# Kernel optimization log

Hardware: AMD Instinct MI355X
Metric: run time of the kernel (lower is better)

The kernel has to match this reference:

```python
import jax, jax.numpy as jnp
import numpy as np
import math

D_MODEL = 1024
NHEAD = 16
HEAD_DIM = D_MODEL // NHEAD  # 64
R_HEAD = 8  # r // nhead = 128 // 16


def setup_inputs() -> dict:
    key = jax.random.key(0)
    ks = jax.random.split(key, 6)
    b, s = 2, 2048
    scale = 1.0 / math.sqrt(D_MODEL)
    return {
        "x": jax.random.normal(ks[0], (b, s, D_MODEL), dtype=jnp.float32),
        "Wq": jax.random.normal(ks[1], (D_MODEL, D_MODEL), dtype=jnp.float32) * scale,
        "Wk": jax.random.normal(ks[2], (D_MODEL, D_MODEL), dtype=jnp.float32) * scale,
        "Wv": jax.random.normal(ks[3], (D_MODEL, D_MODEL), dtype=jnp.float32) * scale,
        "Wo": jax.random.normal(ks[4], (D_MODEL, D_MODEL), dtype=jnp.float32) * scale,
        "B": jax.random.normal(ks[5], (D_MODEL, R_HEAD), dtype=jnp.float32),
    }


def reference(x, Wq, Wk, Wv, Wo, B):
    b, s, d = x.shape
    # Linear projections (torch nn.Linear: y = x @ W.T)
    Q = (x @ Wq.T).reshape(b, s, NHEAD, HEAD_DIM).transpose(0, 2, 1, 3)  # [b,h,s,hd]
    K = (x @ Wk.T).reshape(b, s, NHEAD, HEAD_DIM).transpose(0, 2, 1, 3)
    V = (x @ Wv.T).reshape(b, s, NHEAD, HEAD_DIM).transpose(0, 2, 1, 3)
    # Shared basis: head h uses rows [h*head_dim : (h+1)*head_dim] of B
    B_heads = B.reshape(NHEAD, HEAD_DIM, R_HEAD)  # [h,hd,r]
    # Low-rank projected queries/keys (vectorized form of the per-head loop)
    Qr = jnp.einsum('bhsd,hdr->bhsr', Q, B_heads)  # [b,h,s,r]
    Kr = jnp.einsum('bhsd,hdr->bhsr', K, B_heads)
    scores = jnp.einsum('bhqr,bhkr->bhqk', Qr, Kr) / math.sqrt(R_HEAD)  # [b,h,s,s]
    attn = jax.nn.softmax(scores, axis=-1)  # dropout is identity in eval
    out = jnp.einsum('bhqk,bhkd->bhqd', attn, V)  # [b,h,s,hd]
    out = out.transpose(0, 2, 1, 3).reshape(b, s, d)
    return out @ Wo.T
```

## Files before the change

### kernel.cpp

```cpp
#include <hip/hip_runtime.h>

#define SEQ 2048
#define DM 1024

typedef __attribute__((ext_vector_type(8))) short bs8;
typedef __attribute__((ext_vector_type(4))) float vf4;
typedef __attribute__((ext_vector_type(4))) unsigned int vu4;

__device__ __forceinline__ unsigned short bf16u(float f) {
  unsigned int u = __float_as_uint(f);
  u = (u + 0x7fffu + ((u >> 16) & 1u)) >> 16;
  return (unsigned short)u;
}

__device__ __forceinline__ unsigned int cvt_pk(float lo, float hi) {
  unsigned int r;
  asm("v_cvt_pk_bf16_f32 %0, %1, %2" : "=v"(r) : "v"(lo), "v"(hi));
  return r;
}

__device__ __forceinline__ float fexp2(float x) {
  float r;
  asm("v_exp_f32 %0, %1" : "=v"(r) : "v"(x));
  return r;
}

__device__ __forceinline__ void gload16(const unsigned short* g, unsigned short* l) {
  __builtin_amdgcn_global_load_lds(
      (const __attribute__((address_space(1))) unsigned int*)g,
      (__attribute__((address_space(3))) unsigned int*)l, 16, 0, 0);
}

__global__ void k_combine(const float* __restrict__ Wq, const float* __restrict__ Wk,
                          const float* __restrict__ Bm,
                          unsigned short* __restrict__ Ch, unsigned short* __restrict__ Cl) {
  int e = blockIdx.x * 256 + threadIdx.x;
  int which = e >> 17;
  int rem = e & 131071;
  int hr = rem >> 10;
  int j = rem & 1023;
  int h = hr >> 3, r = hr & 7;
  const float* W = which ? Wk : Wq;
  float acc = 0.f;
  #pragma unroll 8
  for (int d = 0; d < 64; d++) {
    int gd = h * 64 + d;
    acc += Bm[gd * 8 + r] * W[gd * 1024 + j];
  }
  size_t idx = (size_t)(which * 128 + hr) * 1024 + j;
  unsigned short h16 = bf16u(acc);
  float hf = __uint_as_float(((unsigned int)h16) << 16);
  Ch[idx] = h16;
  Cl[idx] = bf16u(acc - hf);
}

__global__ void k_cvt(const float* __restrict__ in, unsigned short* __restrict__ out, int n4) {
  int i = blockIdx.x * 256 + threadIdx.x;
  if (i >= n4) return;
  float4 v = ((const float4*)in)[i];
  ushort4 o;
  o.x = bf16u(v.x); o.y = bf16u(v.y); o.z = bf16u(v.z); o.w = bf16u(v.w);
  ((ushort4*)out)[i] = o;
}

__global__ void k_cvt_hl(const float* __restrict__ in, unsigned short* __restrict__ oh,
                         unsigned short* __restrict__ ol, int n4) {
  int i = blockIdx.x * 256 + threadIdx.x;
  if (i >= n4) return;
  float4 v = ((const float4*)in)[i];
  float f[4] = {v.x, v.y, v.z, v.w};
  ushort4 hv, lv;
  unsigned short hs[4], ls[4];
  #pragma unroll
  for (int j = 0; j < 4; j++) {
    unsigned short h16 = bf16u(f[j]);
    float hf = __uint_as_float(((unsigned int)h16) << 16);
    hs[j] = h16;
    ls[j] = bf16u(f[j] - hf);
  }
  hv.x = hs[0]; hv.y = hs[1]; hv.z = hs[2]; hv.w = hs[3];
  lv.x = ls[0]; lv.y = ls[1]; lv.z = ls[2]; lv.w = ls[3];
  ((ushort4*)oh)[i] = hv;
  ((ushort4*)ol)[i] = lv;
}

__global__ __launch_bounds__(256) void k_qkr(
    const unsigned short* __restrict__ Xh, const unsigned short* __restrict__ Xl,
    const unsigned short* __restrict__ Bh_, const unsigned short* __restrict__ Bl_,
    float* __restrict__ C0, float* __restrict__ C1) {
  const int K = 1024, N = 256;
  __shared__ unsigned short Sah[64 * 64];
  __shared__ unsigned short Sal[64 * 64];
  __shared__ unsigned short Sbh[64 * 64];
  __shared__ unsigned short Sbl[64 * 64];
  int t = threadIdx.x, lane = t & 63, w = t >> 6;
  int gg = lane >> 4, r = lane & 15;
  int m0 = blockIdx.x * 64, n0 = blockIdx.y * 64;
  int kz = blockIdx.z;
  float* C = kz ? C1 : C0;
  vf4 acc[4];
  #pragma unroll
  for (int fn = 0; fn < 4; fn++) acc[fn] = (vf4){0.f, 0.f, 0.f, 0.f};

  int prow = lane >> 3, pslot = lane & 7;
  const unsigned short *ah_src[2], *al_src[2], *bh_src[2], *bl_src[2];
  unsigned short *ah_dst[2], *al_dst[2], *bh_dst[2], *bl_dst[2];
  #pragma unroll
  for (int p = 0; p < 2; p++) {
    int rr = w * 16 + p * 8 + prow;
    int c = pslot ^ ((rr ^ (rr >> 3)) & 7);
    size_t ga = (size_t)(m0 + rr) * K + (size_t)kz * 512 + c * 8;
    ah_src[p] = Xh + ga;  al_src[p] = Xl + ga;
    size_t gb = (size_t)(n0 + rr) * K + (size_t)kz * 512 + c * 8;
    bh_src[p] = Bh_ + gb; bl_src[p] = Bl_ + gb;
    int ldo = (w * 16 + p * 8) * 64;
    ah_dst[p] = &Sah[ldo]; al_dst[p] = &Sal[ldo];
    bh_dst[p] = &Sbh[ldo]; bl_dst[p] = &Sbl[ldo];
  }

  int aoff[2], boff[4][2];
  {
    int arow = w * 16 + r;
    int key = (arow ^ (arow >> 3)) & 7;
    #pragma unroll
    for (int kk = 0; kk < 2; kk++) aoff[kk] = arow * 64 + ((kk * 4 + gg) ^ key) * 8;
  }
  #pragma unroll
  for (int fn = 0; fn < 4; fn++) {
    int brow = fn * 16 + r;
    int key = (brow ^ (brow >> 3)) & 7;
    #pragma unroll
    for (int kk = 0; kk < 2; kk++) boff[fn][kk] = brow * 64 + ((kk * 4 + gg) ^ key) * 8;
  }

  for (int k0 = 0; k0 < 512; k0 += 64) {
    __syncthreads();
    #pragma unroll
    for (int p = 0; p < 2; p++) {
      gload16(ah_src[p] + k0, ah_dst[p]);
      gload16(al_src[p] + k0, al_dst[p]);
      gload16(bh_src[p] + k0, bh_dst[p]);
      gload16(bl_src[p] + k0, bl_dst[p]);
    }
    __syncthreads();
    bs8 afh[2], afl[2], bfh[4][2], bfl[4][2];
    #pragma unroll
    for (int kk = 0; kk < 2; kk++) {
      afh[kk] = *(const bs8*)&Sah[aoff[kk]];
      afl[kk] = *(const bs8*)&Sal[aoff[kk]];
    }
    #pragma unroll
    for (int fn = 0; fn < 4; fn++)
      #pragma unroll
      for (int kk = 0; kk < 2; kk++) {
        bfh[fn][kk] = *(const bs8*)&Sbh[boff[fn][kk]];
        bfl[fn][kk] = *(const bs8*)&Sbl[boff[fn][kk]];
      }
    #pragma unroll
    for (int kk = 0; kk < 2; kk++)
      #pragma unroll
      for (int fn = 0; fn < 4; fn++) {
        acc[fn] = __builtin_amdgcn_mfma_f32_16x16x32_bf16(afh[kk], bfh[fn][kk], acc[fn], 0, 0, 0);
        acc[fn] = __builtin_amdgcn_mfma_f32_16x16x32_bf16(afh[kk], bfl[fn][kk], acc[fn], 0, 0, 0);
        acc[fn] = __builtin_amdgcn_mfma_f32_16x16x32_bf16(afl[kk], bfh[fn][kk], acc[fn], 0, 0, 0);
      }
  }

  #pragma unroll
  for (int fn = 0; fn < 4; fn++)
    #pragma unroll
    for (int j = 0; j < 4; j++) {
      int m = m0 + w * 16 + gg * 4 + j;
      int n = n0 + fn * 16 + r;
      C[(size_t)m * N + n] = acc[fn][j];
    }
}

__global__ void k_hilo(const float* __restrict__ QA, const float* __restrict__ QB,
                       unsigned short* __restrict__ Qhl, unsigned short* __restrict__ Khl) {
  int i = blockIdx.x * 256 + threadIdx.x;
  int side = i >> 16;
  int nh = i & 65535;
  int n = nh & 4095;
  int h = nh >> 12;
  size_t off = (size_t)n * 256 + side * 128 + h * 8;
  const float sc = side ? 1.0f : (1.4426950408889634f * 0.35355339059327373f);
  unsigned short* dst = (side ? Khl : Qhl) + ((size_t)h * 4096 + n) * 16;
  float4 a0 = *(const float4*)&QA[off];
  float4 a1 = *(const float4*)&QA[off + 4];
  float4 b0 = *(const float4*)&QB[off];
  float4 b1 = *(const float4*)&QB[off + 4];
  float f[8] = {a0.x+b0.x, a0.y+b0.y, a0.z+b0.z, a0.w+b0.w,
                a1.x+b1.x, a1.y+b1.y, a1.z+b1.z, a1.w+b1.w};
  unsigned short hs[8], ls[8];
  #pragma unroll
  for (int j = 0; j < 8; j++) {
    float fs = f[j] * sc;
    unsigned short h16 = bf16u(fs);
    float hf = __uint_as_float(((unsigned int)h16) << 16);
    hs[j] = h16;
    ls[j] = bf16u(fs - hf);
  }
  uint4 hv = {(unsigned int)hs[0] | ((unsigned int)hs[1] << 16),
              (unsigned int)hs[2] | ((unsigned int)hs[3] << 16),
              (unsigned int)hs[4] | ((unsigned int)hs[5] << 16),
              (unsigned int)hs[6] | ((unsigned int)hs[7] << 16)};
  uint4 lv = {(unsigned int)ls[0] | ((unsigned int)ls[1] << 16),
              (unsigned int)ls[2] | ((unsigned int)ls[3] << 16),
              (unsigned int)ls[4] | ((unsigned int)ls[5] << 16),
              (unsigned int)ls[6] | ((unsigned int)ls[7] << 16)};
  *(uint4*)dst = hv;
  *(uint4*)(dst + 8) = lv;
}

template<int OUT>
__global__ __launch_bounds__(256) void k_gemm128(const unsigned short* __restrict__ A,
    const unsigned short* __restrict__ W, void* __restrict__ Cout, int M, int N, int K) {
  __shared__ unsigned short Ah[128 * 64];
  __shared__ unsigned short Bh[64 * 64];
  int t = threadIdx.x, lane = t & 63, w = t >> 6;
  int gg = lane >> 4, r = lane & 15;
  int m0 = blockIdx.x * 128, n0 = blockIdx.y * 64;
  vf4 acc[2][4];
  #pragma unroll
  for (int i = 0; i < 2; i++)
    #pragma unroll
    for (int j = 0; j < 4; j++) acc[i][j] = (vf4){0.f, 0.f, 0.f, 0.f};

  int prow = lane >> 3, pslot = lane & 7;
  const unsigned short* asrc[4];
  unsigned short* aldst[4];
  #pragma unroll
  for (int p = 0; p < 4; p++) {
    int rr = w * 32 + p * 8 + prow;
    int c = pslot ^ ((rr ^ (rr >> 3)) & 7);
    asrc[p] = &A[(size_t)(m0 + rr) * K + c * 8];
    aldst[p] = &Ah[(w * 32 + p * 8) * 64];
  }
  const unsigned short* bsrc[2];
  unsigned short* bldst[2];
  #pragma unroll
  for (int p = 0; p < 2; p++) {
    int rn = w * 16 + p * 8 + prow;
    int c = pslot ^ ((rn ^ (rn >> 3)) & 7);
    bsrc[p] = &W[(size_t)(n0 + rn) * K + c * 8];
    bldst[p] = &Bh[(w * 16 + p * 8) * 64];
  }

  int aoff[2][2], boff[4][2];
  #pragma unroll
  for (int fm = 0; fm < 2; fm++) {
    int arow = w * 32 + fm * 16 + r;
    int key = (arow ^ (arow >> 3)) & 7;
    #pragma unroll
    for (int kk = 0; kk < 2; kk++)
      aoff[fm][kk] = arow * 64 + ((kk * 4 + gg) ^ key) * 8;
  }
  #pragma unroll
  for (int fn = 0; fn < 4; fn++) {
    int brow = fn * 16 + r;
    int key = (brow ^ (brow >> 3)) & 7;
    #pragma unroll
    for (int kk = 0; kk < 2; kk++)
      boff[fn][kk] = brow * 64 + ((kk * 4 + gg) ^ key) * 8;
  }

  for (int k0 = 0; k0 < K; k0 += 64) {
    __syncthreads();
    #pragma unroll
    for (int p = 0; p < 4; p++) gload16(asrc[p] + k0, aldst[p]);
    #pragma unroll
    for (int p = 0; p < 2; p++) gload16(bsrc[p] + k0, bldst[p]);
    __syncthreads();
    bs8 af[2][2], bf[4][2];
    #pragma unroll
    for (int fm = 0; fm < 2; fm++)
      #pragma unroll
      for (int kk = 0; kk < 2; kk++) af[fm][kk] = *(const bs8*)&Ah[aoff[fm][kk]];
    #pragma unroll
    for (int fn = 0; fn < 4; fn++)
      #pragma unroll
      for (int kk = 0; kk < 2; kk++) bf[fn][kk] = *(const bs8*)&Bh[boff[fn][kk]];
    #pragma unroll
    for (int kk = 0; kk < 2; kk++)
      #pragma unroll
      for (int fm = 0; fm < 2; fm++)
        #pragma unroll
        for (int fn = 0; fn < 4; fn++)
          acc[fm][fn] = __builtin_amdgcn_mfma_f32_16x16x32_bf16(af[fm][kk], bf[fn][kk], acc[fm][fn], 0, 0, 0);
  }

  #pragma unroll
  for (int fm = 0; fm < 2; fm++)
    #pragma unroll
    for (int fn = 0; fn < 4; fn++) {
      if (OUT == 2) {
        int n = n0 + fn * 16 + r;
        int m = m0 + w * 32 + fm * 16 + gg * 4;
        ushort4 st = {bf16u(acc[fm][fn][0]), bf16u(acc[fm][fn][1]),
                      bf16u(acc[fm][fn][2]), bf16u(acc[fm][fn][3])};
        *(ushort4*)&((unsigned short*)Cout)[(size_t)n * M + m] = st;
      } else {
        #pragma unroll
        for (int j = 0; j < 4; j++) {
          int m = m0 + w * 32 + fm * 16 + gg * 4 + j;
          int n = n0 + fn * 16 + r;
          ((float*)Cout)[(size_t)m * N + n] = acc[fm][fn][j];
        }
      }
    }
}

__global__ __launch_bounds__(256, 4) void k_attn(const unsigned short* __restrict__ Qhl,
    const unsigned short* __restrict__ Khl, const unsigned short* __restrict__ Vt,
    unsigned short* __restrict__ AO) {
  int bx = blockIdx.x;
  int qt = bx & 31, h = (bx >> 5) & 15, b = bx >> 9;
  int t = threadIdx.x, lane = t & 63, w = t >> 6;
  int gg = lane >> 4, r = lane & 15;

  __shared__ unsigned short VT[2][4096];

  int qglob = b * 2048 + qt * 64 + w * 16 + r;
  bs8 bq = {0, 0, 0, 0, 0, 0, 0, 0};
  if (gg != 3)
    bq = *(const bs8*)&Qhl[((size_t)h * 4096 + qglob) * 16 + (gg == 2 ? 8 : 0)];

  const unsigned short* Khead = &Khl[((size_t)h * 4096 + (size_t)b * 2048) * 16];
  int koff = (gg == 1) ? 8 : 0;
  const unsigned short* kp[4];
  #pragma unroll
  for (int kt = 0; kt < 4; kt++) {
    int ks = (kt & 1) * 32 + (r >> 2) * 8 + (kt >> 1) * 4 + (r & 3);
    kp[kt] = Khead + (size_t)ks * 16 + koff;
  }

  int vrow = t >> 2, vcl = t & 3;
  const unsigned short* vsrc = &Vt[(size_t)(h * 64 + vrow) * 4096 + (size_t)b * 2048 + vcl * 16];
  int vkey = (vrow ^ (vrow >> 2)) & 7;
  int sw0 = ((vcl * 2) ^ vkey) * 8;
  int sw1 = ((vcl * 2 + 1) ^ vkey) * 8;

  int pvoff[2][4];
  #pragma unroll
  for (int sl = 0; sl < 2; sl++)
    #pragma unroll
    for (int fn = 0; fn < 4; fn++) {
      int row = 4 * r + fn;
      int key = (row ^ (row >> 2)) & 7;
      pvoff[sl][fn] = row * 64 + ((sl * 4 + gg) ^ key) * 8;
    }

  float mrun = -INFINITY;
  vf4 acc[4];
  #pragma unroll
  for (int i = 0; i < 4; i++) acc[i] = (vf4){0.f, 0.f, 0.f, 0.f};
  vf4 accs = (vf4){0.f, 0.f, 0.f, 0.f};

  const bs8 ones = (bs8){16256, 16256, 16256, 16256, 16256, 16256, 16256, 16256};

  uint4 fv0 = *(const uint4*)(vsrc);
  uint4 fv1 = *(const uint4*)(vsrc + 8);
  bs8 af0 = *(const bs8*)(kp[0]);
  bs8 af1 = *(const bs8*)(kp[1]);
  bs8 af2 = *(const bs8*)(kp[2]);
  bs8 af3 = *(const bs8*)(kp[3]);
  {
    unsigned short* vd = &VT[0][vrow * 64];
    *(uint4*)(vd + sw0) = fv0;
    *(uint4*)(vd + sw1) = fv1;
  }
  __syncthreads();

  #pragma unroll 2
  for (int kc = 0; kc < 32; kc++) {
    int nc = kc < 31 ? kc + 1 : 31;
    uint4 nv0 = *(const uint4*)(vsrc + nc * 64);
    uint4 nv1 = *(const uint4*)(vsrc + nc * 64 + 8);
    size_t nb16 = (size_t)nc * 64 * 16;
    bs8 naf0 = *(const bs8*)(kp[0] + nb16);
    bs8 naf1 = *(const bs8*)(kp[1] + nb16);
    bs8 naf2 = *(const bs8*)(kp[2] + nb16);
    bs8 naf3 = *(const bs8*)(kp[3] + nb16);

    vf4 z = (vf4){0.f, 0.f, 0.f, 0.f};
    __builtin_amdgcn_s_setprio(1);
    vf4 s0 = __builtin_amdgcn_mfma_f32_16x16x32_bf16(af0, bq, z, 0, 0, 0);
    vf4 s1 = __builtin_amdgcn_mfma_f32_16x16x32_bf16(af1, bq, z, 0, 0, 0);
    vf4 s2 = __builtin_amdgcn_mfma_f32_16x16x32_bf16(af2, bq, z, 0, 0, 0);
    vf4 s3 = __builtin_amdgcn_mfma_f32_16x16x32_bf16(af3, bq, z, 0, 0, 0);
    __builtin_amdgcn_s_setprio(0);

    float p[16];
    #pragma unroll
    for (int j = 0; j < 4; j++) {
      p[0 + j] = s0[j]; p[4 + j] = s1[j]; p[8 + j] = s2[j]; p[12 + j] = s3[j];
    }
    float cm0 = fmaxf(fmaxf(p[0],  p[1]),  p[2]);
    float cm1 = fmaxf(fmaxf(p[3],  p[4]),  p[5]);
    float cm2 = fmaxf(fmaxf(p[6],  p[7]),  p[8]);
    float cm3 = fmaxf(fmaxf(p[9],  p[10]), p[11]);
    float cm4 = fmaxf(fmaxf(p[12], p[13]), p[14]);
    float cmax = fmaxf(fmaxf(fmaxf(cm0, cm1), cm2),
                       fmaxf(fmaxf(cm3, cm4), p[15]));
    cmax = fmaxf(cmax, __shfl_xor(cmax, 16));
    cmax = fmaxf(cmax, __shfl_xor(cmax, 32));

    if (!__all(cmax <= mrun + 8.f)) {
      float mnew = fmaxf(mrun, cmax);
      float alpha = fexp2(mrun - mnew);
      float al[4];
      #pragma unroll
      for (int j = 0; j < 4; j++) al[j] = __shfl(alpha, gg * 4 + j);
      #pragma unroll
      for (int fn = 0; fn < 4; fn++) {
        acc[fn][0] *= al[0]; acc[fn][1] *= al[1];
        acc[fn][2] *= al[2]; acc[fn][3] *= al[3];
      }
      accs[0] *= al[0]; accs[1] *= al[1];
      accs[2] *= al[2]; accs[3] *= al[3];
      mrun = mnew;
    }

    #pragma unroll
    for (int i = 0; i < 16; i++) p[i] = fexp2(p[i] - mrun);

    vu4 a0 = {cvt_pk(p[0],  p[1]),  cvt_pk(p[2],  p[3]),
              cvt_pk(p[8],  p[9]),  cvt_pk(p[10], p[11])};
    vu4 a1 = {cvt_pk(p[4],  p[5]),  cvt_pk(p[6],  p[7]),
              cvt_pk(p[12], p[13]), cvt_pk(p[14], p[15])};
    bs8 apv0 = __builtin_bit_cast(bs8, a0);
    bs8 apv1 = __builtin_bit_cast(bs8, a1);

    const unsigned short* vb = &VT[kc & 1][0];
    __builtin_amdgcn_s_setprio(1);
    #pragma unroll
    for (int sl = 0; sl < 2; sl++) {
      bs8 a = sl ? apv1 : apv0;
      #pragma unroll
      for (int fn = 0; fn < 4; fn++) {
        bs8 bv = *(const bs8*)&vb[pvoff[sl][fn]];
        acc[fn] = __builtin_amdgcn_mfma_f32_16x16x32_bf16(a, bv, acc[fn], 0, 0, 0);
      }
    }
    accs = __builtin_amdgcn_mfma_f32_16x16x32_bf16(apv0, ones, accs, 0, 0, 0);
    accs = __builtin_amdgcn_mfma_f32_16x16x32_bf16(apv1, ones, accs, 0, 0, 0);
    __builtin_amdgcn_s_setprio(0);

    af0 = naf0; af1 = naf1; af2 = naf2; af3 = naf3;

    if (kc < 31) {
      unsigned short* vd = &VT[(kc + 1) & 1][vrow * 64];
      *(uint4*)(vd + sw0) = nv0;
      *(uint4*)(vd + sw1) = nv1;
      __syncthreads();
    }
  }

  float li[4];
  #pragma unroll
  for (int j = 0; j < 4; j++) li[j] = 1.f / accs[j];
  #pragma unroll
  for (int j = 0; j < 4; j++) {
    uint2 o;
    o.x = cvt_pk(acc[0][j] * li[j], acc[1][j] * li[j]);
    o.y = cvt_pk(acc[2][j] * li[j], acc[3][j] * li[j]);
    int qq = qt * 64 + w * 16 + gg * 4 + j;
    *(uint2*)&AO[((size_t)b * SEQ + qq) * 1024 + h * 64 + 4 * r] = o;
  }
}

extern "C" void kernel_launch(void* const* d_in, const int* in_sizes, int n_in,
                              void* d_out, int out_size, void* d_ws, size_t ws_size,
                              hipStream_t stream) {
  const float* x  = (const float*)d_in[0];
  const float* Wq = (const float*)d_in[1];
  const float* Wk = (const float*)d_in[2];
  const float* Wv = (const float*)d_in[3];
  const float* Wo = (const float*)d_in[4];
  const float* Bm = (const float*)d_in[5];
  float* out = (float*)d_out;

  char* ws = (char*)d_ws;
  unsigned short* Cqkh = (unsigned short*)ws;  ws += (size_t)256 * 1024 * 2;
  unsigned short* Cqkl = (unsigned short*)ws;  ws += (size_t)256 * 1024 * 2;
  float* QKrA = (float*)ws;                    ws += (size_t)4096 * 256 * 4;
  float* QKrB = (float*)ws;                    ws += (size_t)4096 * 256 * 4;
  unsigned short* xh  = (unsigned short*)ws;   ws += (size_t)4096 * 1024 * 2;
  unsigned short* Wvh = (unsigned short*)ws;   ws += (size_t)1024 * 1024 * 2;
  unsigned short* Woh = (unsigned short*)ws;   ws += (size_t)1024 * 1024 * 2;
  unsigned short* Vt  = (unsigned short*)ws;   ws += (size_t)4096 * 1024 * 2;
  unsigned short* AO  = (unsigned short*)ws;   ws += (size_t)4096 * 1024 * 2;
  unsigned short* Qhl = (unsigned short*)ws;   ws += (size_t)16 * 4096 * 16 * 2;
  unsigned short* Khl = (unsigned short*)ws;   ws += (size_t)16 * 4096 * 16 * 2;
  unsigned short* xl = AO;

  k_combine<<<1024, 256, 0, stream>>>(Wq, Wk, Bm, Cqkh, Cqkl);
  k_cvt_hl<<<4096, 256, 0, stream>>>(x, xh, xl, 1048576);
  k_cvt<<<1024, 256, 0, stream>>>(Wv, Wvh, 262144);
  k_cvt<<<1024, 256, 0, stream>>>(Wo, Woh, 262144);
  k_qkr<<<dim3(64, 4, 2), 256, 0, stream>>>(xh, xl, Cqkh, Cqkl, QKrA, QKrB);
  k_hilo<<<512, 256, 0, stream>>>(QKrA, QKrB, Qhl, Khl);
  k_gemm128<2><<<dim3(32, 16), 256, 0, stream>>>(xh, Wvh, (void*)Vt, 4096, 1024, 1024);
  k_attn<<<1024, 256, 0, stream>>>(Qhl, Khl, Vt, AO);
  k_gemm128<0><<<dim3(32, 16), 256, 0, stream>>>(AO, Woh, (void*)out, 4096, 1024, 1024);
}
```

Baseline: 118.1 us.

## Split attention key range across two wave groups with LDS merge

The attention kernel now launches 512 threads per block. Two groups of four waves each process half of the key sequence for the same 64 queries, using separate double-buffered V tiles in shared memory. At the end, group 1 writes its running max, row sums and partial accumulators to LDS, and group 0 rescales and combines them online-softmax style before writing the output. This halves the serial key loop per wave and raises wave-level parallelism. The costs are an extra LDS round-trip and barrier, doubled shared memory per block, and a launch bound of (512,8) that may squeeze the register budget.

New measurement: 276.1 us. 2.34x slower.

```diff
diff --git a/kernel.cpp b/kernel.cpp
--- a/kernel.cpp
+++ b/kernel.cpp
@@ -311,22 +311,24 @@
     }
 }
 
-__global__ __launch_bounds__(256, 4) void k_attn(const unsigned short* __restrict__ Qhl,
+__global__ __launch_bounds__(512, 8) void k_attn(const unsigned short* __restrict__ Qhl,
     const unsigned short* __restrict__ Khl, const unsigned short* __restrict__ Vt,
     unsigned short* __restrict__ AO) {
   int bx = blockIdx.x;
   int qt = bx & 31, h = (bx >> 5) & 15, b = bx >> 9;
   int t = threadIdx.x, lane = t & 63, w = t >> 6;
+  int kvg = w >> 2, wq = w & 3;
   int gg = lane >> 4, r = lane & 15;
 
-  __shared__ unsigned short VT[2][4096];
-
-  int qglob = b * 2048 + qt * 64 + w * 16 + r;
+  __shared__ unsigned short VT[2][2][4096];
+
+  int qglob = b * 2048 + qt * 64 + wq * 16 + r;
   bs8 bq = {0, 0, 0, 0, 0, 0, 0, 0};
   if (gg != 3)
     bq = *(const bs8*)&Qhl[((size_t)h * 4096 + qglob) * 16 + (gg == 2 ? 8 : 0)];
 
-  const unsigned short* Khead = &Khl[((size_t)h * 4096 + (size_t)b * 2048) * 16];
+  const unsigned short* Khead = &Khl[((size_t)h * 4096 + (size_t)b * 2048) * 16]
+                                + (size_t)kvg * 16 * 64 * 16;
   int koff = (gg == 1) ? 8 : 0;
   const unsigned short* kp[4];
   #pragma unroll
@@ -335,8 +337,10 @@
     kp[kt] = Khead + (size_t)ks * 16 + koff;
   }
 
-  int vrow = t >> 2, vcl = t & 3;
-  const unsigned short* vsrc = &Vt[(size_t)(h * 64 + vrow) * 4096 + (size_t)b * 2048 + vcl * 16];
+  int tg = t & 255;
+  int vrow = tg >> 2, vcl = tg & 3;
+  const unsigned short* vsrc = &Vt[(size_t)(h * 64 + vrow) * 4096 + (size_t)b * 2048
+                                   + (size_t)kvg * 16 * 64 + vcl * 16];
   int vkey = (vrow ^ (vrow >> 2)) & 7;
   int sw0 = ((vcl * 2) ^ vkey) * 8;
   int sw1 = ((vcl * 2 + 1) ^ vkey) * 8;
@@ -366,15 +370,15 @@
   bs8 af2 = *(const bs8*)(kp[2]);
   bs8 af3 = *(const bs8*)(kp[3]);
   {
-    unsigned short* vd = &VT[0][vrow * 64];
+    unsigned short* vd = &VT[kvg][0][vrow * 64];
     *(uint4*)(vd + sw0) = fv0;
     *(uint4*)(vd + sw1) = fv1;
   }
   __syncthreads();
 
   #pragma unroll 2
-  for (int kc = 0; kc < 32; kc++) {
-    int nc = kc < 31 ? kc + 1 : 31;
+  for (int kc = 0; kc < 16; kc++) {
+    int nc = kc < 15 ? kc + 1 : 15;
     uint4 nv0 = *(const uint4*)(vsrc + nc * 64);
     uint4 nv1 = *(const uint4*)(vsrc + nc * 64 + 8);
     size_t nb16 = (size_t)nc * 64 * 16;
@@ -432,7 +436,7 @@
     bs8 apv0 = __builtin_bit_cast(bs8, a0);
     bs8 apv1 = __builtin_bit_cast(bs8, a1);
 
-    const unsigned short* vb = &VT[kc & 1][0];
+    const unsigned short* vb = &VT[kvg][kc & 1][0];
     __builtin_amdgcn_s_setprio(1);
     #pragma unroll
     for (int sl = 0; sl < 2; sl++) {
@@ -449,13 +453,52 @@
 
     af0 = naf0; af1 = naf1; af2 = naf2; af3 = naf3;
 
-    if (kc < 31) {
-      unsigned short* vd = &VT[(kc + 1) & 1][vrow * 64];
+    if (kc < 15) {
+      unsigned short* vd = &VT[kvg][(kc + 1) & 1][vrow * 64];
       *(uint4*)(vd + sw0) = nv0;
       *(uint4*)(vd + sw1) = nv1;
       __syncthreads();
     }
   }
+
+  __syncthreads();
+  float* Lbase = (float*)&VT[0][0][0];
+  float* Lm = Lbase;
+  float* Ll = Lbase + 64;
+  float* La = Lbase + 128;
+  if (kvg == 1) {
+    if (gg == 0) Lm[wq * 16 + r] = mrun;
+    if (r == 0) {
+      #pragma unroll
+      for (int j = 0; j < 4; j++) Ll[wq * 16 + gg * 4 + j] = accs[j];
+    }
+    float* dst = &La[(wq * 64 + lane) * 20];
+    #pragma unroll
+    for (int fn = 0; fn < 4; fn++) *(vf4*)(dst + fn * 4) = acc[fn];
+  }
+  __syncthreads();
+  if (kvg == 1) return;
+
+  float m1 = Lm[wq * 16 + r];
+  float mx = fmaxf(mrun, m1);
+  float e0 = fexp2(mrun - mx), e1 = fexp2(m1 - mx);
+  float al0[4], al1[4], l1[4];
+  #pragma unroll
+  for (int j = 0; j < 4; j++) {
+    al0[j] = __shfl(e0, gg * 4 + j);
+    al1[j] = __shfl(e1, gg * 4 + j);
+    l1[j] = Ll[wq * 16 + gg * 4 + j];
+  }
+  const float* src = &La[(wq * 64 + lane) * 20];
+  #pragma unroll
+  for (int fn = 0; fn < 4; fn++) {
+    vf4 o1 = *(const vf4*)(src + fn * 4);
+    #pragma unroll
+    for (int j = 0; j < 4; j++)
+      acc[fn][j] = acc[fn][j] * al0[j] + o1[j] * al1[j];
+  }
+  #pragma unroll
+  for (int j = 0; j < 4; j++) accs[j] = accs[j] * al0[j] + l1[j] * al1[j];
 
   float li[4];
   #pragma unroll
@@ -465,7 +508,7 @@
     uint2 o;
     o.x = cvt_pk(acc[0][j] * li[j], acc[1][j] * li[j]);
     o.y = cvt_pk(acc[2][j] * li[j], acc[3][j] * li[j]);
-    int qq = qt * 64 + w * 16 + gg * 4 + j;
+    int qq = qt * 64 + wq * 16 + gg * 4 + j;
     *(uint2*)&AO[((size_t)b * SEQ + qq) * 1024 + h * 64 + 4 * r] = o;
   }
 }
@@ -502,6 +545,6 @@
   k_qkr<<<dim3(64, 4, 2), 256, 0, stream>>>(xh, xl, Cqkh, Cqkl, QKrA, QKrB);
   k_hilo<<<512, 256, 0, stream>>>(QKrA, QKrB, Qhl, Khl);
   k_gemm128<2><<<dim3(32, 16), 256, 0, stream>>>(xh, Wvh, (void*)Vt, 4096, 1024, 1024);
-  k_attn<<<1024, 256, 0, stream>>>(Qhl, Khl, Vt, AO);
+  k_attn<<<1024, 512, 0, stream>>>(Qhl, Khl, Vt, AO);
   k_gemm128<0><<<dim3(32, 16), 256, 0, stream>>>(AO, Woh, (void*)out, 4096, 1024, 1024);
 }
```
